# Kernel optimization log

Hardware: AMD Instinct MI355X
Metric: run time of the kernel (lower is better)

The kernel has to match this reference:

```python
import jax, jax.numpy as jnp
import numpy as np

NI, ND, NH = 128, 32, 4  # feature dim, head dim, n heads


def setup_inputs() -> dict:
    key = jax.random.key(0)
    ks = jax.random.split(key, 8)
    nb, nloc, nnei = 2, 1024, 120
    g1 = jax.random.normal(ks[0], (nb, nloc, NI), dtype=jnp.float32)
    gg1 = jax.random.normal(ks[1], (nb, nloc, nnei, NI), dtype=jnp.float32)
    nlist_mask = jax.random.randint(ks[2], (nb, nloc, nnei), 0, 2) > 0
    sw = jax.random.uniform(ks[3], (nb, nloc, nnei), dtype=jnp.float32)
    s = 1.0 / np.sqrt(NI)
    Wq = jax.random.normal(ks[4], (NI, ND * NH), dtype=jnp.float32) * s
    Wkv = jax.random.normal(ks[5], (NI, (ND + NI) * NH), dtype=jnp.float32) * s
    Wh = jax.random.normal(ks[6], (NI * NH, NI), dtype=jnp.float32) * (1.0 / np.sqrt(NI * NH))
    bh = jax.random.normal(ks[7], (NI,), dtype=jnp.float32) * 0.01
    return {"g1": g1, "gg1": gg1, "nlist_mask": nlist_mask, "sw": sw,
            "Wq": Wq, "Wkv": Wkv, "Wh": Wh, "bh": bh}


def reference(g1, gg1, nlist_mask, sw, Wq, Wkv, Wh, bh):
    nb, nloc, nnei = nlist_mask.shape
    # q: [nb, nloc, nh, nd]
    q = (g1 @ Wq).reshape(nb, nloc, ND, NH).transpose(0, 1, 3, 2)
    # kv: [nb, nloc, nh, nnei, nd+ni]
    kv = (gg1 @ Wkv).reshape(nb, nloc, nnei, ND + NI, NH).transpose(0, 1, 4, 2, 3)
    k = kv[..., :ND]   # [nb, nloc, nh, nnei, nd]
    v = kv[..., ND:]   # [nb, nloc, nh, nnei, ni]
    # attention logits over neighbors: [nb, nloc, nh, nnei]
    attnw = jnp.einsum("blhd,blhjd->blhj", q, k) / np.sqrt(ND).astype(np.float32)
    mask = nlist_mask[:, :, None, :]  # [nb, nloc, 1, nnei]
    attnw = jnp.where(mask, attnw, -jnp.inf)
    attnw = jax.nn.softmax(attnw, axis=-1)
    attnw = jnp.where(mask, attnw, 0.0)
    attnw = attnw * sw[:, :, None, :]  # smoothing weight
    ret = jnp.einsum("blhj,blhji->blhi", attnw, v).reshape(nb, nloc, NH * NI)
    return ret @ Wh + bh
```

## Files before the change

### kernel.cpp

```cpp
#include <hip/hip_runtime.h>
#include <math.h>

#define NI   128
#define ND   32
#define NH   4
#define NNEI 120
#define KVW  640
#define NCOL 512

template<int CTRL>
__device__ __forceinline__ float dppf(float x) {
    return __int_as_float(__builtin_amdgcn_update_dpp(
        0, __float_as_int(x), CTRL, 0xF, 0xF, true));
}
__device__ __forceinline__ float red16_sum(float x) {
    x += dppf<0xB1>(x);
    x += dppf<0x4E>(x);
    x += dppf<0x141>(x);
    x += dppf<0x140>(x);
    return x;
}
__device__ __forceinline__ float red16_max(float x) {
    x = fmaxf(x, dppf<0xB1>(x));
    x = fmaxf(x, dppf<0x4E>(x));
    x = fmaxf(x, dppf<0x141>(x));
    x = fmaxf(x, dppf<0x140>(x));
    return x;
}

__global__ __launch_bounds__(256)
void precompute_MP(const float* __restrict__ Wq, const float* __restrict__ Wkv,
                   const float* __restrict__ Wh, float* __restrict__ M2, float* __restrict__ P2)
{
    int idx = blockIdx.x * 256 + threadIdx.x;
    if (idx < NI * NCOL) {
        int i  = idx & 127;
        int h  = (idx >> 7) & 3;
        int i2 = idx >> 9;
        float acc = 0.f;
        #pragma unroll 8
        for (int d = 0; d < ND; ++d)
            acc += Wq[i2 * NI + d * NH + h] * Wkv[i * KVW + d * NH + h];
        M2[i2 * NCOL + h * NI + i] = acc * 0.17677669529663687f;
    } else {
        int j  = idx - NI * NCOL;
        int io = j & 127;
        int i  = (j >> 7) & 127;
        int h  = j >> 14;
        float acc = 0.f;
        #pragma unroll 8
        for (int iv = 0; iv < NI; ++iv)
            acc += Wkv[i * KVW + (ND + iv) * NH + h] * Wh[(h * NI + iv) * NI + io];
        P2[j] = acc;
    }
}

template<int BM, int BN, int BK, int TM, int TN, bool BIAS>
__global__ __launch_bounds__(256)
void gemm_kernel(const float* __restrict__ A, const float* __restrict__ B,
                 const float* __restrict__ bias, float* __restrict__ C,
                 int M, int N, int K)
{
    __shared__ float As[BK][BM + 4];
    __shared__ float Bs[BK][BN + 4];
    const int tid = threadIdx.x;
    const int nbx = N / BN;
    const int bx = blockIdx.x % nbx, by = blockIdx.x / nbx;
    const int m0 = by * BM, n0 = bx * BN;
    const int tx = tid & 15, ty = tid >> 4;

    constexpr int LA = BM * BK / (4 * 256);
    constexpr int LB = BK * BN / (4 * 256);
    constexpr int AF4 = BK / 4;
    constexpr int BF4 = BN / 4;

    float acc[TM][TN] = {};

    for (int k0 = 0; k0 < K; k0 += BK) {
        #pragma unroll
        for (int p = 0; p < LA; ++p) {
            int u  = tid + p * 256;
            int r  = u / AF4;
            int c4 = u % AF4;
            float4 v = *(const float4*)(A + (size_t)(m0 + r) * K + k0 + c4 * 4);
            As[c4 * 4 + 0][r] = v.x;
            As[c4 * 4 + 1][r] = v.y;
            As[c4 * 4 + 2][r] = v.z;
            As[c4 * 4 + 3][r] = v.w;
        }
        #pragma unroll
        for (int p = 0; p < LB; ++p) {
            int u  = tid + p * 256;
            int kk = u / BF4;
            int c4 = u % BF4;
            float4 v = *(const float4*)(B + (size_t)(k0 + kk) * N + n0 + c4 * 4);
            *(float4*)&Bs[kk][c4 * 4] = v;
        }
        __syncthreads();
        #pragma unroll
        for (int kk = 0; kk < BK; ++kk) {
            float a[TM], b[TN];
            if constexpr (TM == 4) {
                float4 a4 = *(const float4*)&As[kk][ty * 4];
                a[0] = a4.x; a[1] = a4.y; a[2] = a4.z; a[3] = a4.w;
            } else {
                #pragma unroll
                for (int m = 0; m < TM; ++m) a[m] = As[kk][ty * TM + m];
            }
            if constexpr (TN == 4) {
                float4 b4 = *(const float4*)&Bs[kk][tx * 4];
                b[0] = b4.x; b[1] = b4.y; b[2] = b4.z; b[3] = b4.w;
            } else {
                #pragma unroll
                for (int n = 0; n < TN; ++n) b[n] = Bs[kk][tx * TN + n];
            }
            #pragma unroll
            for (int m = 0; m < TM; ++m)
                #pragma unroll
                for (int n = 0; n < TN; ++n)
                    acc[m][n] += a[m] * b[n];
        }
        __syncthreads();
    }
    #pragma unroll
    for (int m = 0; m < TM; ++m) {
        int mm = m0 + ty * TM + m;
        #pragma unroll
        for (int n = 0; n < TN; ++n) {
            int nn = n0 + tx * TN + n;
            C[(size_t)mm * N + nn] = acc[m][n] + (BIAS ? bias[nn] : 0.f);
        }
    }
}

__device__ __forceinline__ bool load_mask(const void* p, int is_i32, int idx) {
    if (is_i32) return ((const int*)p)[idx] != 0;
    return ((const unsigned char*)p)[idx] != 0;
}

__global__ __launch_bounds__(256, 3)
void atten_kernel(const float* __restrict__ gg1, const float* __restrict__ qW_all,
                  const void* __restrict__ mask_raw, const float* __restrict__ sw,
                  float* __restrict__ t_all)
{
    __shared__ float  s_logit[NH][NNEI];
    __shared__ float  s_attn[NH][NNEI];
    __shared__ float4 s_part2[16][NH][33];
    __shared__ int    s_is_i32;

    const int tid  = threadIdx.x;
    const int bl   = blockIdx.x;
    const int w    = tid >> 6;
    const int lane = tid & 63;
    const int q    = lane >> 4;
    const int c    = lane & 15;

    if (tid < 64) {
        unsigned v = ((const unsigned*)mask_raw)[tid];
        unsigned long long b = __ballot(v <= 1u);
        if (tid == 0) s_is_i32 = (b == 0xFFFFFFFFFFFFFFFFull) ? 1 : 0;
    }

    const float4* gbase = (const float4*)(gg1 + (size_t)bl * NNEI * NI);
    float4 rgA[8], rgB[8];
    #pragma unroll
    for (int t = 0; t < 8; ++t) {
        int j  = 16 * t + 4 * q + w;
        int jc = (j < NNEI) ? j : 0;
        rgA[t] = gbase[jc * 32 + c];
        rgB[t] = gbase[jc * 32 + c + 16];
    }

    const float4* qwbase = (const float4*)(qW_all + (size_t)bl * NCOL);
    float4 qwA[NH], qwB[NH];
    #pragma unroll
    for (int h = 0; h < NH; ++h) {
        qwA[h] = qwbase[h * 32 + c];
        qwB[h] = qwbase[h * 32 + c + 16];
    }

    #pragma unroll
    for (int t = 0; t < 8; ++t) {
        float4 gA = rgA[t], gB = rgB[t];
        float s0, s1, s2, s3;
        s0 = qwA[0].x*gA.x + qwA[0].y*gA.y + qwA[0].z*gA.z + qwA[0].w*gA.w
           + qwB[0].x*gB.x + qwB[0].y*gB.y + qwB[0].z*gB.z + qwB[0].w*gB.w;
        s1 = qwA[1].x*gA.x + qwA[1].y*gA.y + qwA[1].z*gA.z + qwA[1].w*gA.w
           + qwB[1].x*gB.x + qwB[1].y*gB.y + qwB[1].z*gB.z + qwB[1].w*gB.w;
        s2 = qwA[2].x*gA.x + qwA[2].y*gA.y + qwA[2].z*gA.z + qwA[2].w*gA.w
           + qwB[2].x*gB.x + qwB[2].y*gB.y + qwB[2].z*gB.z + qwB[2].w*gB.w;
        s3 = qwA[3].x*gA.x + qwA[3].y*gA.y + qwA[3].z*gA.z + qwA[3].w*gA.w
           + qwB[3].x*gB.x + qwB[3].y*gB.y + qwB[3].z*gB.z + qwB[3].w*gB.w;
        s0 = red16_sum(s0);
        s1 = red16_sum(s1);
        s2 = red16_sum(s2);
        s3 = red16_sum(s3);
        int j = 16 * t + 4 * q + w;
        if (c == 0 && j < NNEI) {
            s_logit[0][j] = s0;
            s_logit[1][j] = s1;
            s_logit[2][j] = s2;
            s_logit[3][j] = s3;
        }
    }
    __syncthreads();

    {
        const int h  = w;
        const int j0 = lane, j1 = lane + 64;
        const int j1c = (j1 < NNEI) ? j1 : 0;
        bool m0 = load_mask(mask_raw, s_is_i32, bl * NNEI + j0);
        bool m1 = (j1 < NNEI) && load_mask(mask_raw, s_is_i32, bl * NNEI + j1c);
        float v0 = m0 ? s_logit[h][j0] : -INFINITY;
        float v1 = m1 ? s_logit[h][j1c] : -INFINITY;

        float mx = fmaxf(v0, v1);
        mx = red16_max(mx);
        mx = fmaxf(mx, __shfl_xor(mx, 16));
        mx = fmaxf(mx, __shfl_xor(mx, 32));

        float e0 = 0.f, e1 = 0.f;
        if (mx != -INFINITY) {
            e0 = m0 ? __expf(v0 - mx) : 0.f;
            e1 = m1 ? __expf(v1 - mx) : 0.f;
        }
        float s = e0 + e1;
        s = red16_sum(s);
        s += __shfl_xor(s, 16);
        s += __shfl_xor(s, 32);
        float inv = (s > 0.f) ? (1.f / s) : 0.f;

        s_attn[h][j0] = e0 * inv * sw[bl * NNEI + j0];
        if (j1 < NNEI) s_attn[h][j1] = e1 * inv * sw[bl * NNEI + j1];
    }
    __syncthreads();

    {
        float4 aA[NH] = {{0,0,0,0},{0,0,0,0},{0,0,0,0},{0,0,0,0}};
        float4 aB[NH] = {{0,0,0,0},{0,0,0,0},{0,0,0,0},{0,0,0,0}};
        #pragma unroll
        for (int t = 0; t < 8; ++t) {
            int j = 16 * t + 4 * q + w;
            bool val = (j < NNEI);
            float4 gA = rgA[t], gB = rgB[t];
            #pragma unroll
            for (int h = 0; h < NH; ++h) {
                float a = val ? s_attn[h][j] : 0.f;
                aA[h].x += a * gA.x; aA[h].y += a * gA.y;
                aA[h].z += a * gA.z; aA[h].w += a * gA.w;
                aB[h].x += a * gB.x; aB[h].y += a * gB.y;
                aB[h].z += a * gB.z; aB[h].w += a * gB.w;
            }
        }
        #pragma unroll
        for (int h = 0; h < NH; ++h) {
            s_part2[w * 4 + q][h][c]      = aA[h];
            s_part2[w * 4 + q][h][c + 16] = aB[h];
        }
    }
    __syncthreads();

    if (tid < 128) {
        int h = tid >> 5, cc = tid & 31;
        float4 r = {0.f, 0.f, 0.f, 0.f};
        #pragma unroll
        for (int g = 0; g < 16; ++g) {
            float4 v = s_part2[g][h][cc];
            r.x += v.x; r.y += v.y; r.z += v.z; r.w += v.w;
        }
        ((float4*)(t_all + (size_t)bl * NCOL + h * NI))[cc] = r;
    }
}

__global__ __launch_bounds__(256, 2)
void fused_fallback(const float* __restrict__ g1, const float* __restrict__ gg1,
                    const void* __restrict__ mask_raw, const float* __restrict__ sw,
                    const float* __restrict__ M2, const float* __restrict__ P2,
                    const float* __restrict__ bh, float* __restrict__ out)
{
    __shared__ float s_gg[NNEI * 129];
    __shared__ float s_qW[NH][NI];
    __shared__ float s_attn[NH][NNEI];
    __shared__ float s_t[NH][NI];
    __shared__ float s_part[2][NI];
    __shared__ int   s_is_i32;

    const int tid = threadIdx.x;
    const int bl  = blockIdx.x;

    if (tid < 64) {
        unsigned v = ((const unsigned*)mask_raw)[tid];
        unsigned long long b = __ballot(v <= 1u);
        if (tid == 0) s_is_i32 = (b == 0xFFFFFFFFFFFFFFFFull) ? 1 : 0;
    }
    {
        const float4* gsrc = (const float4*)(gg1 + (size_t)bl * NNEI * NI);
        #pragma unroll
        for (int p = 0; p < 15; ++p) {
            int u = tid + p * 256;
            int r = u >> 5, c4 = u & 31;
            float4 v = gsrc[u];
            float* dst = &s_gg[r * 129 + c4 * 4];
            dst[0] = v.x; dst[1] = v.y; dst[2] = v.z; dst[3] = v.w;
        }
    }
    {
        const float* g1r = g1 + bl * NI;
        #pragma unroll
        for (int p = 0; p < 2; ++p) {
            int o = tid + p * 256;
            int i = o & (NI - 1);
            int h = o >> 7;
            const float* Mp = M2 + h * NI + i;
            float acc = 0.f;
            #pragma unroll 8
            for (int i2 = 0; i2 < NI; ++i2) acc += g1r[i2] * Mp[i2 * NCOL];
            s_qW[h][i] = acc;
        }
    }
    __syncthreads();
    {
        const int lane = tid & 63, h = tid >> 6;
        const int j0 = lane, j1 = lane + 64;
        const int j1c = (j1 < NNEI) ? j1 : 0;
        const float* row0 = &s_gg[j0 * 129];
        const float* row1 = &s_gg[j1c * 129];
        float dot0 = 0.f, dot1 = 0.f;
        #pragma unroll 8
        for (int i = 0; i < NI; ++i) {
            float w = s_qW[h][i];
            dot0 += row0[i] * w;
            dot1 += row1[i] * w;
        }
        bool m0 = load_mask(mask_raw, s_is_i32, bl * NNEI + j0);
        bool m1 = (j1 < NNEI) && load_mask(mask_raw, s_is_i32, bl * NNEI + j1c);
        float v0 = m0 ? dot0 : -INFINITY;
        float v1 = m1 ? dot1 : -INFINITY;
        float mx = fmaxf(v0, v1);
        #pragma unroll
        for (int off = 32; off; off >>= 1) mx = fmaxf(mx, __shfl_xor(mx, off));
        float e0 = 0.f, e1 = 0.f;
        if (mx != -INFINITY) {
            e0 = m0 ? __expf(v0 - mx) : 0.f;
            e1 = m1 ? __expf(v1 - mx) : 0.f;
        }
        float s = e0 + e1;
        #pragma unroll
        for (int off = 32; off; off >>= 1) s += __shfl_xor(s, off);
        float inv = (s > 0.f) ? (1.f / s) : 0.f;
        s_attn[h][j0] = e0 * inv * sw[bl * NNEI + j0];
        if (j1 < NNEI) s_attn[h][j1] = e1 * inv * sw[bl * NNEI + j1];
    }
    __syncthreads();
    #pragma unroll
    for (int p = 0; p < 2; ++p) {
        int o = tid + p * 256;
        int i = o & (NI - 1);
        int h = o >> 7;
        float acc = 0.f;
        #pragma unroll 8
        for (int j = 0; j < NNEI; ++j) acc += s_attn[h][j] * s_gg[j * 129 + i];
        s_t[h][i] = acc;
    }
    __syncthreads();
    {
        int io = tid & (NI - 1);
        int half = tid >> 7;
        float acc = 0.f;
        #pragma unroll 2
        for (int h = half * 2; h < half * 2 + 2; ++h) {
            const float* Pp = P2 + h * NI * NI + io;
            #pragma unroll 8
            for (int i = 0; i < NI; ++i) acc += s_t[h][i] * Pp[i * NI];
        }
        s_part[half][io] = acc;
    }
    __syncthreads();
    if (tid < NI)
        out[bl * NI + tid] = s_part[0][tid] + s_part[1][tid] + bh[tid];
}

extern "C" void kernel_launch(void* const* d_in, const int* in_sizes, int n_in,
                              void* d_out, int out_size, void* d_ws, size_t ws_size,
                              hipStream_t stream) {
    const float* g1   = (const float*)d_in[0];
    const float* gg1  = (const float*)d_in[1];
    const void*  mask = d_in[2];
    const float* sw   = (const float*)d_in[3];
    const float* Wq   = (const float*)d_in[4];
    const float* Wkv  = (const float*)d_in[5];
    const float* Wh   = (const float*)d_in[6];
    const float* bh   = (const float*)d_in[7];
    float* out = (float*)d_out;

    const int nbl = in_sizes[0] / NI;
    const size_t nM = (size_t)NI * NCOL;
    const size_t nP = (size_t)NCOL * NI;
    const size_t nQ = (size_t)nbl * NCOL;

    float* M2 = (float*)d_ws;
    float* P2 = M2 + nM;

    precompute_MP<<<512, 256, 0, stream>>>(Wq, Wkv, Wh, M2, P2);

    if (ws_size >= (nM + nP + 2 * nQ) * sizeof(float)) {
        float* qW = P2 + nP;
        float* tA = qW + nQ;
        gemm_kernel<64, 64, 32, 4, 4, false>
            <<<(nbl / 64) * (NCOL / 64), 256, 0, stream>>>(g1, M2, nullptr, qW, nbl, NCOL, NI);
        atten_kernel<<<nbl, 256, 0, stream>>>(gg1, qW, mask, sw, tA);
        gemm_kernel<16, 64, 64, 1, 4, true>
            <<<(nbl / 16) * (NI / 64), 256, 0, stream>>>(tA, P2, bh, out, nbl, NI, NCOL);
    } else {
        fused_fallback<<<nbl, 256, 0, stream>>>(g1, gg1, mask, sw, M2, P2, bh, out);
    }
}
```

Measured before the change: 62.25 us.

## Fuse q-projection, attention and output GEMM into one multi-atom kernel

```diff
diff --git a/kernel.cpp b/kernel.cpp
--- a/kernel.cpp
+++ b/kernel.cpp
@@ -7,6 +7,7 @@
 #define NNEI 120
 #define KVW  640
 #define NCOL 512
+#define ATOMS 4
 
 template<int CTRL>
 __device__ __forceinline__ float dppf(float x) {
@@ -55,128 +56,41 @@
     }
 }
 
-template<int BM, int BN, int BK, int TM, int TN, bool BIAS>
-__global__ __launch_bounds__(256)
-void gemm_kernel(const float* __restrict__ A, const float* __restrict__ B,
-                 const float* __restrict__ bias, float* __restrict__ C,
-                 int M, int N, int K)
-{
-    __shared__ float As[BK][BM + 4];
-    __shared__ float Bs[BK][BN + 4];
-    const int tid = threadIdx.x;
-    const int nbx = N / BN;
-    const int bx = blockIdx.x % nbx, by = blockIdx.x / nbx;
-    const int m0 = by * BM, n0 = bx * BN;
-    const int tx = tid & 15, ty = tid >> 4;
-
-    constexpr int LA = BM * BK / (4 * 256);
-    constexpr int LB = BK * BN / (4 * 256);
-    constexpr int AF4 = BK / 4;
-    constexpr int BF4 = BN / 4;
-
-    float acc[TM][TN] = {};
-
-    for (int k0 = 0; k0 < K; k0 += BK) {
-        #pragma unroll
-        for (int p = 0; p < LA; ++p) {
-            int u  = tid + p * 256;
-            int r  = u / AF4;
-            int c4 = u % AF4;
-            float4 v = *(const float4*)(A + (size_t)(m0 + r) * K + k0 + c4 * 4);
-            As[c4 * 4 + 0][r] = v.x;
-            As[c4 * 4 + 1][r] = v.y;
-            As[c4 * 4 + 2][r] = v.z;
-            As[c4 * 4 + 3][r] = v.w;
-        }
-        #pragma unroll
-        for (int p = 0; p < LB; ++p) {
-            int u  = tid + p * 256;
-            int kk = u / BF4;
-            int c4 = u % BF4;
-            float4 v = *(const float4*)(B + (size_t)(k0 + kk) * N + n0 + c4 * 4);
-            *(float4*)&Bs[kk][c4 * 4] = v;
-        }
-        __syncthreads();
-        #pragma unroll
-        for (int kk = 0; kk < BK; ++kk) {
-            float a[TM], b[TN];
-            if constexpr (TM == 4) {
-                float4 a4 = *(const float4*)&As[kk][ty * 4];
-                a[0] = a4.x; a[1] = a4.y; a[2] = a4.z; a[3] = a4.w;
-            } else {
-                #pragma unroll
-                for (int m = 0; m < TM; ++m) a[m] = As[kk][ty * TM + m];
-            }
-            if constexpr (TN == 4) {
-                float4 b4 = *(const float4*)&Bs[kk][tx * 4];
-                b[0] = b4.x; b[1] = b4.y; b[2] = b4.z; b[3] = b4.w;
-            } else {
-                #pragma unroll
-                for (int n = 0; n < TN; ++n) b[n] = Bs[kk][tx * TN + n];
-            }
-            #pragma unroll
-            for (int m = 0; m < TM; ++m)
-                #pragma unroll
-                for (int n = 0; n < TN; ++n)
-                    acc[m][n] += a[m] * b[n];
-        }
-        __syncthreads();
-    }
-    #pragma unroll
-    for (int m = 0; m < TM; ++m) {
-        int mm = m0 + ty * TM + m;
-        #pragma unroll
-        for (int n = 0; n < TN; ++n) {
-            int nn = n0 + tx * TN + n;
-            C[(size_t)mm * N + nn] = acc[m][n] + (BIAS ? bias[nn] : 0.f);
-        }
-    }
-}
-
 __device__ __forceinline__ bool load_mask(const void* p, int is_i32, int idx) {
     if (is_i32) return ((const int*)p)[idx] != 0;
     return ((const unsigned char*)p)[idx] != 0;
 }
 
-__global__ __launch_bounds__(256, 3)
-void atten_kernel(const float* __restrict__ gg1, const float* __restrict__ qW_all,
-                  const void* __restrict__ mask_raw, const float* __restrict__ sw,
-                  float* __restrict__ t_all)
-{
-    __shared__ float  s_logit[NH][NNEI];
-    __shared__ float  s_attn[NH][NNEI];
-    __shared__ float4 s_part2[16][NH][33];
-    __shared__ int    s_is_i32;
-
-    const int tid  = threadIdx.x;
-    const int bl   = blockIdx.x;
-    const int w    = tid >> 6;
-    const int lane = tid & 63;
-    const int q    = lane >> 4;
-    const int c    = lane & 15;
-
-    if (tid < 64) {
-        unsigned v = ((const unsigned*)mask_raw)[tid];
-        unsigned long long b = __ballot(v <= 1u);
-        if (tid == 0) s_is_i32 = (b == 0xFFFFFFFFFFFFFFFFull) ? 1 : 0;
-    }
-
-    const float4* gbase = (const float4*)(gg1 + (size_t)bl * NNEI * NI);
-    float4 rgA[8], rgB[8];
+__device__ __forceinline__ void load_rows(const float4* gbase, int w, int q, int c,
+                                          float4 (&A)[8], float4 (&B)[8]) {
     #pragma unroll
     for (int t = 0; t < 8; ++t) {
         int j  = 16 * t + 4 * q + w;
         int jc = (j < NNEI) ? j : 0;
-        rgA[t] = gbase[jc * 32 + c];
-        rgB[t] = gbase[jc * 32 + c + 16];
-    }
-
-    const float4* qwbase = (const float4*)(qW_all + (size_t)bl * NCOL);
+        A[t] = gbase[jc * 32 + c];
+        B[t] = gbase[jc * 32 + c + 16];
+    }
+}
+
+__device__ __forceinline__ void atom_body(
+    int bl, int tid, int w, int lane, int q, int c, int is_i32,
+    const float4 (&rgA)[8], const float4 (&rgB)[8],
+    const float4* s_qW4a, float (*s_logit)[NNEI], float (*s_attn)[NNEI],
+    float4* s_scr, float4* s_t4a,
+    const void* __restrict__ mask_raw, const float* __restrict__ sw)
+{
+    const int j0 = lane, j1 = lane + 64;
+    const int j1c = (j1 < NNEI) ? j1 : 0;
+    bool m0 = load_mask(mask_raw, is_i32, bl * NNEI + j0);
+    bool m1 = (j1 < NNEI) && load_mask(mask_raw, is_i32, bl * NNEI + j1c);
+    float sw0 = sw[bl * NNEI + j0];
+    float sw1 = (j1 < NNEI) ? sw[bl * NNEI + j1] : 0.f;
+
     float4 qwA[NH], qwB[NH];
     #pragma unroll
     for (int h = 0; h < NH; ++h) {
-        qwA[h] = qwbase[h * 32 + c];
-        qwB[h] = qwbase[h * 32 + c + 16];
+        qwA[h] = s_qW4a[h * 32 + c];
+        qwB[h] = s_qW4a[h * 32 + c + 16];
     }
 
     #pragma unroll
@@ -206,19 +120,12 @@
     __syncthreads();
 
     {
-        const int h  = w;
-        const int j0 = lane, j1 = lane + 64;
-        const int j1c = (j1 < NNEI) ? j1 : 0;
-        bool m0 = load_mask(mask_raw, s_is_i32, bl * NNEI + j0);
-        bool m1 = (j1 < NNEI) && load_mask(mask_raw, s_is_i32, bl * NNEI + j1c);
-        float v0 = m0 ? s_logit[h][j0] : -INFINITY;
-        float v1 = m1 ? s_logit[h][j1c] : -INFINITY;
-
+        float v0 = m0 ? s_logit[w][j0] : -INFINITY;
+        float v1 = m1 ? s_logit[w][j1c] : -INFINITY;
         float mx = fmaxf(v0, v1);
         mx = red16_max(mx);
         mx = fmaxf(mx, __shfl_xor(mx, 16));
         mx = fmaxf(mx, __shfl_xor(mx, 32));
-
         float e0 = 0.f, e1 = 0.f;
         if (mx != -INFINITY) {
             e0 = m0 ? __expf(v0 - mx) : 0.f;
@@ -229,15 +136,13 @@
         s += __shfl_xor(s, 16);
         s += __shfl_xor(s, 32);
         float inv = (s > 0.f) ? (1.f / s) : 0.f;
-
-        s_attn[h][j0] = e0 * inv * sw[bl * NNEI + j0];
-        if (j1 < NNEI) s_attn[h][j1] = e1 * inv * sw[bl * NNEI + j1];
-    }
-    __syncthreads();
-
-    {
-        float4 aA[NH] = {{0,0,0,0},{0,0,0,0},{0,0,0,0},{0,0,0,0}};
-        float4 aB[NH] = {{0,0,0,0},{0,0,0,0},{0,0,0,0},{0,0,0,0}};
+        s_attn[w][j0] = e0 * inv * sw0;
+        if (j1 < NNEI) s_attn[w][j1] = e1 * inv * sw1;
+    }
+    __syncthreads();
+
+    {
+        float4 aA[NH] = {}, aB[NH] = {};
         #pragma unroll
         for (int t = 0; t < 8; ++t) {
             int j = 16 * t + 4 * q + w;
@@ -252,10 +157,11 @@
                 aB[h].z += a * gB.z; aB[h].w += a * gB.w;
             }
         }
+        int grp = w * 4 + q;
         #pragma unroll
         for (int h = 0; h < NH; ++h) {
-            s_part2[w * 4 + q][h][c]      = aA[h];
-            s_part2[w * 4 + q][h][c + 16] = aB[h];
+            s_scr[grp * 132 + h * 33 + c]      = aA[h];
+            s_scr[grp * 132 + h * 33 + c + 16] = aB[h];
         }
     }
     __syncthreads();
@@ -265,10 +171,130 @@
         float4 r = {0.f, 0.f, 0.f, 0.f};
         #pragma unroll
         for (int g = 0; g < 16; ++g) {
-            float4 v = s_part2[g][h][cc];
+            float4 v = s_scr[g * 132 + h * 33 + cc];
             r.x += v.x; r.y += v.y; r.z += v.z; r.w += v.w;
         }
-        ((float4*)(t_all + (size_t)bl * NCOL + h * NI))[cc] = r;
+        s_t4a[h * 32 + cc] = r;
+    }
+    __syncthreads();
+}
+
+__global__ __launch_bounds__(256, 2)
+void fused_atten(const float* __restrict__ g1, const float* __restrict__ gg1,
+                 const void* __restrict__ mask_raw, const float* __restrict__ sw,
+                 const float* __restrict__ M2, const float* __restrict__ P2,
+                 const float* __restrict__ bh, float* __restrict__ out)
+{
+    __shared__ float  s_g1[ATOMS][NI];
+    __shared__ float4 s_qW4[ATOMS][NI];
+    __shared__ float  s_logit[NH][NNEI];
+    __shared__ float  s_attn[NH][NNEI];
+    __shared__ float4 s_t4[ATOMS][NI];
+    __shared__ float4 s_scr[2112];
+    __shared__ int    s_is_i32;
+
+    const int tid  = threadIdx.x;
+    const int bl0  = blockIdx.x * ATOMS;
+    const int w    = tid >> 6;
+    const int lane = tid & 63;
+    const int q    = lane >> 4;
+    const int c    = lane & 15;
+
+    if (tid < 64) {
+        unsigned v = ((const unsigned*)mask_raw)[tid];
+        unsigned long long b = __ballot(v <= 1u);
+        if (tid == 0) s_is_i32 = (b == 0xFFFFFFFFFFFFFFFFull) ? 1 : 0;
+    }
+    if (tid < ATOMS * NI / 4)
+        ((float4*)s_g1)[tid] = ((const float4*)(g1 + (size_t)bl0 * NI))[tid];
+
+    const float4* gb0 = (const float4*)(gg1 + (size_t)(bl0 + 0) * NNEI * NI);
+    const float4* gb1 = (const float4*)(gg1 + (size_t)(bl0 + 1) * NNEI * NI);
+    const float4* gb2 = (const float4*)(gg1 + (size_t)(bl0 + 2) * NNEI * NI);
+    const float4* gb3 = (const float4*)(gg1 + (size_t)(bl0 + 3) * NNEI * NI);
+    float4 rA0[8], rB0[8], rA1[8], rB1[8];
+    load_rows(gb0, w, q, c, rA0, rB0);
+    load_rows(gb1, w, q, c, rA1, rB1);
+
+    __syncthreads();
+    const int is_i32 = s_is_i32;
+
+    {
+        const int col4 = tid & 127, halfk = tid >> 7;
+        float4 acc[ATOMS] = {};
+        const float4* M2_4 = (const float4*)M2;
+        #pragma unroll 8
+        for (int it = 0; it < 64; ++it) {
+            int i2 = it * 2 + halfk;
+            float4 m = M2_4[i2 * 128 + col4];
+            #pragma unroll
+            for (int a = 0; a < ATOMS; ++a) {
+                float gv = s_g1[a][i2];
+                acc[a].x += gv * m.x; acc[a].y += gv * m.y;
+                acc[a].z += gv * m.z; acc[a].w += gv * m.w;
+            }
+        }
+        #pragma unroll
+        for (int a = 0; a < ATOMS; ++a)
+            s_scr[(halfk * ATOMS + a) * 129 + col4] = acc[a];
+    }
+    __syncthreads();
+    {
+        #pragma unroll
+        for (int e = 0; e < 2; ++e) {
+            int idx = tid + e * 256;
+            int a = idx >> 7, c4 = idx & 127;
+            float4 x = s_scr[a * 129 + c4];
+            float4 y = s_scr[(4 + a) * 129 + c4];
+            float4 r; r.x = x.x + y.x; r.y = x.y + y.y; r.z = x.z + y.z; r.w = x.w + y.w;
+            s_qW4[a][c4] = r;
+        }
+    }
+    __syncthreads();
+
+    atom_body(bl0 + 0, tid, w, lane, q, c, is_i32, rA0, rB0,
+              &s_qW4[0][0], s_logit, s_attn, s_scr, &s_t4[0][0], mask_raw, sw);
+    load_rows(gb2, w, q, c, rA0, rB0);
+    atom_body(bl0 + 1, tid, w, lane, q, c, is_i32, rA1, rB1,
+              &s_qW4[1][0], s_logit, s_attn, s_scr, &s_t4[1][0], mask_raw, sw);
+    load_rows(gb3, w, q, c, rA1, rB1);
+    atom_body(bl0 + 2, tid, w, lane, q, c, is_i32, rA0, rB0,
+              &s_qW4[2][0], s_logit, s_attn, s_scr, &s_t4[2][0], mask_raw, sw);
+    atom_body(bl0 + 3, tid, w, lane, q, c, is_i32, rA1, rB1,
+              &s_qW4[3][0], s_logit, s_attn, s_scr, &s_t4[3][0], mask_raw, sw);
+
+    {
+        const int io4 = tid & 31, g = tid >> 5;
+        float4 oacc[ATOMS] = {};
+        const float4* P2_4 = (const float4*)P2;
+        const float*  s_tf = (const float*)s_t4;
+        #pragma unroll 8
+        for (int it = 0; it < 64; ++it) {
+            int kk = it * 8 + g;
+            float4 p = P2_4[kk * 32 + io4];
+            #pragma unroll
+            for (int a = 0; a < ATOMS; ++a) {
+                float tv = s_tf[a * NCOL + kk];
+                oacc[a].x += tv * p.x; oacc[a].y += tv * p.y;
+                oacc[a].z += tv * p.z; oacc[a].w += tv * p.w;
+            }
+        }
+        #pragma unroll
+        for (int a = 0; a < ATOMS; ++a)
+            s_scr[(g * ATOMS + a) * 33 + io4] = oacc[a];
+    }
+    __syncthreads();
+    if (tid < 128) {
+        int a = tid >> 5, io4 = tid & 31;
+        float4 r = {0.f, 0.f, 0.f, 0.f};
+        #pragma unroll
+        for (int g = 0; g < 8; ++g) {
+            float4 v = s_scr[(g * ATOMS + a) * 33 + io4];
+            r.x += v.x; r.y += v.y; r.z += v.z; r.w += v.w;
+        }
+        float4 b = ((const float4*)bh)[io4];
+        r.x += b.x; r.y += b.y; r.z += b.z; r.w += b.w;
+        ((float4*)out)[(size_t)(bl0 + a) * 32 + io4] = r;
     }
 }
 
@@ -396,21 +422,14 @@
     const int nbl = in_sizes[0] / NI;
     const size_t nM = (size_t)NI * NCOL;
     const size_t nP = (size_t)NCOL * NI;
-    const size_t nQ = (size_t)nbl * NCOL;
 
     float* M2 = (float*)d_ws;
     float* P2 = M2 + nM;
 
     precompute_MP<<<512, 256, 0, stream>>>(Wq, Wkv, Wh, M2, P2);
 
-    if (ws_size >= (nM + nP + 2 * nQ) * sizeof(float)) {
-        float* qW = P2 + nP;
-        float* tA = qW + nQ;
-        gemm_kernel<64, 64, 32, 4, 4, false>
-            <<<(nbl / 64) * (NCOL / 64), 256, 0, stream>>>(g1, M2, nullptr, qW, nbl, NCOL, NI);
-        atten_kernel<<<nbl, 256, 0, stream>>>(gg1, qW, mask, sw, tA);
-        gemm_kernel<16, 64, 64, 1, 4, true>
-            <<<(nbl / 16) * (NI / 64), 256, 0, stream>>>(tA, P2, bh, out, nbl, NI, NCOL);
+    if ((nbl % ATOMS) == 0) {
+        fused_atten<<<nbl / ATOMS, 256, 0, stream>>>(g1, gg1, mask, sw, M2, P2, bh, out);
     } else {
         fused_fallback<<<nbl, 256, 0, stream>>>(g1, gg1, mask, sw, M2, P2, bh, out);
     }
```

After: 66.01 us. 1.06x slower.

## Shrink attention kernel LDS footprint and raise launch-bounds occupancy target

Applied to the files above, without the earlier changes.

```diff
diff --git a/kernel.cpp b/kernel.cpp
--- a/kernel.cpp
+++ b/kernel.cpp
@@ -138,14 +138,13 @@
     return ((const unsigned char*)p)[idx] != 0;
 }
 
-__global__ __launch_bounds__(256, 3)
+__global__ __launch_bounds__(256, 8)
 void atten_kernel(const float* __restrict__ gg1, const float* __restrict__ qW_all,
                   const void* __restrict__ mask_raw, const float* __restrict__ sw,
                   float* __restrict__ t_all)
 {
-    __shared__ float  s_logit[NH][NNEI];
-    __shared__ float  s_attn[NH][NNEI];
-    __shared__ float4 s_part2[16][NH][33];
+    __shared__ float  s_sm[NH][NNEI];
+    __shared__ float4 s_p8[8][NH][32];
     __shared__ int    s_is_i32;
 
     const int tid  = threadIdx.x;
@@ -197,22 +196,21 @@
         s3 = red16_sum(s3);
         int j = 16 * t + 4 * q + w;
         if (c == 0 && j < NNEI) {
-            s_logit[0][j] = s0;
-            s_logit[1][j] = s1;
-            s_logit[2][j] = s2;
-            s_logit[3][j] = s3;
-        }
-    }
-    __syncthreads();
-
-    {
-        const int h  = w;
+            s_sm[0][j] = s0;
+            s_sm[1][j] = s1;
+            s_sm[2][j] = s2;
+            s_sm[3][j] = s3;
+        }
+    }
+    __syncthreads();
+
+    {
         const int j0 = lane, j1 = lane + 64;
         const int j1c = (j1 < NNEI) ? j1 : 0;
         bool m0 = load_mask(mask_raw, s_is_i32, bl * NNEI + j0);
         bool m1 = (j1 < NNEI) && load_mask(mask_raw, s_is_i32, bl * NNEI + j1c);
-        float v0 = m0 ? s_logit[h][j0] : -INFINITY;
-        float v1 = m1 ? s_logit[h][j1c] : -INFINITY;
+        float v0 = m0 ? s_sm[w][j0] : -INFINITY;
+        float v1 = m1 ? s_sm[w][j1c] : -INFINITY;
 
         float mx = fmaxf(v0, v1);
         mx = red16_max(mx);
@@ -230,14 +228,13 @@
         s += __shfl_xor(s, 32);
         float inv = (s > 0.f) ? (1.f / s) : 0.f;
 
-        s_attn[h][j0] = e0 * inv * sw[bl * NNEI + j0];
-        if (j1 < NNEI) s_attn[h][j1] = e1 * inv * sw[bl * NNEI + j1];
-    }
-    __syncthreads();
-
-    {
-        float4 aA[NH] = {{0,0,0,0},{0,0,0,0},{0,0,0,0},{0,0,0,0}};
-        float4 aB[NH] = {{0,0,0,0},{0,0,0,0},{0,0,0,0},{0,0,0,0}};
+        s_sm[w][j0] = e0 * inv * sw[bl * NNEI + j0];
+        if (j1 < NNEI) s_sm[w][j1] = e1 * inv * sw[bl * NNEI + j1];
+    }
+    __syncthreads();
+
+    {
+        float4 aA[NH] = {}, aB[NH] = {};
         #pragma unroll
         for (int t = 0; t < 8; ++t) {
             int j = 16 * t + 4 * q + w;
@@ -245,17 +242,32 @@
             float4 gA = rgA[t], gB = rgB[t];
             #pragma unroll
             for (int h = 0; h < NH; ++h) {
-                float a = val ? s_attn[h][j] : 0.f;
+                float a = val ? s_sm[h][j] : 0.f;
                 aA[h].x += a * gA.x; aA[h].y += a * gA.y;
                 aA[h].z += a * gA.z; aA[h].w += a * gA.w;
                 aB[h].x += a * gB.x; aB[h].y += a * gB.y;
                 aB[h].z += a * gB.z; aB[h].w += a * gB.w;
             }
         }
-        #pragma unroll
-        for (int h = 0; h < NH; ++h) {
-            s_part2[w * 4 + q][h][c]      = aA[h];
-            s_part2[w * 4 + q][h][c + 16] = aB[h];
+        const int slot = w * 2 + (q & 1);
+        if (q < 2) {
+            #pragma unroll
+            for (int h = 0; h < NH; ++h) {
+                s_p8[slot][h][c]      = aA[h];
+                s_p8[slot][h][c + 16] = aB[h];
+            }
+        }
+        __syncthreads();
+        if (q >= 2) {
+            #pragma unroll
+            for (int h = 0; h < NH; ++h) {
+                float4 v = s_p8[slot][h][c];
+                v.x += aA[h].x; v.y += aA[h].y; v.z += aA[h].z; v.w += aA[h].w;
+                s_p8[slot][h][c] = v;
+                float4 u = s_p8[slot][h][c + 16];
+                u.x += aB[h].x; u.y += aB[h].y; u.z += aB[h].z; u.w += aB[h].w;
+                s_p8[slot][h][c + 16] = u;
+            }
         }
     }
     __syncthreads();
@@ -264,8 +276,8 @@
         int h = tid >> 5, cc = tid & 31;
         float4 r = {0.f, 0.f, 0.f, 0.f};
         #pragma unroll
-        for (int g = 0; g < 16; ++g) {
-            float4 v = s_part2[g][h][cc];
+        for (int g = 0; g < 8; ++g) {
+            float4 v = s_p8[g][h][cc];
             r.x += v.x; r.y += v.y; r.z += v.z; r.w += v.w;
         }
         ((float4*)(t_all + (size_t)bl * NCOL + h * NI))[cc] = r;
```

New measurement: 192.3 us. 3.09x slower.
